# Kernel optimization log

Hardware: AMD Instinct MI355X
Metric: run time of the kernel (lower is better)

The kernel has to match this reference:

```python
import jax, jax.numpy as jnp
import numpy as np

D_MODEL = 1024
NUM_HEADS = 16
D_K = D_MODEL // NUM_HEADS
BATCH = 2
SEQ = 2048


def setup_inputs() -> dict:
    key = jax.random.key(0)
    ks = jax.random.split(key, 11)
    s = 1.0 / np.sqrt(D_MODEL)
    return {
        "query": jax.random.normal(ks[0], (BATCH, SEQ, D_MODEL), jnp.float32),
        "key_": jax.random.normal(ks[1], (BATCH, SEQ, D_MODEL), jnp.float32),
        "value": jax.random.normal(ks[2], (BATCH, SEQ, D_MODEL), jnp.float32),
        "w_q": jax.random.uniform(ks[3], (D_MODEL, D_MODEL), jnp.float32, -s, s),
        "b_q": jax.random.uniform(ks[4], (D_MODEL,), jnp.float32, -s, s),
        "w_k": jax.random.uniform(ks[5], (D_MODEL, D_MODEL), jnp.float32, -s, s),
        "b_k": jax.random.uniform(ks[6], (D_MODEL,), jnp.float32, -s, s),
        "w_v": jax.random.uniform(ks[7], (D_MODEL, D_MODEL), jnp.float32, -s, s),
        "b_v": jax.random.uniform(ks[8], (D_MODEL,), jnp.float32, -s, s),
        "w_o": jax.random.uniform(ks[9], (D_MODEL, D_MODEL), jnp.float32, -s, s),
        "b_o": jax.random.uniform(ks[10], (D_MODEL,), jnp.float32, -s, s),
    }


def reference(query, key_, value, w_q, b_q, w_k, b_k, w_v, b_v, w_o, b_o):
    B, S, D = query.shape
    H, dk = NUM_HEADS, D_K

    def proj(x, w, b):
        # torch Linear: x @ w.T + b ; reshape to (B, H, S, dk)
        return (x @ w.T + b).reshape(B, S, H, dk).transpose(0, 2, 1, 3)

    Q = proj(query, w_q, b_q)
    K = proj(key_, w_k, b_k)
    V = proj(value, w_v, b_v)

    scores = jnp.einsum("bhqd,bhkd->bhqk", Q, K) / jnp.sqrt(jnp.float32(dk))
    attn = jax.nn.softmax(scores, axis=-1)  # dropout is identity in eval
    ctx = jnp.einsum("bhqk,bhkd->bhqd", attn, V)
    ctx = ctx.transpose(0, 2, 1, 3).reshape(B, S, D)
    out = ctx @ w_o.T + b_o
    return out
```

## Files before the change

### kernel.cpp

```cpp
#include <hip/hip_runtime.h>
#include <cstdint>
#include <cstddef>

typedef unsigned short u16;
typedef short bf16x8 __attribute__((ext_vector_type(8)));
typedef unsigned short u16x8 __attribute__((ext_vector_type(8)));
typedef float f32x4 __attribute__((ext_vector_type(4)));

#define NHEAD 16
#define SEQ 2048
#define DMODEL 1024
#define BATCH 2
#define QSCALE 0.18033688011112042f

__device__ __forceinline__ float exp2_fast(float x) {
  return __builtin_amdgcn_exp2f(x);
}

__device__ __forceinline__ u16 f2bf(float f) {
  union { float f; unsigned u; } v; v.f = f;
  return (u16)((v.u + 0x7fffu + ((v.u >> 16) & 1u)) >> 16);
}

__device__ __forceinline__ unsigned cvt_pk(float a, float b) {
  unsigned r;
  asm("v_cvt_pk_bf16_f32 %0, %1, %2" : "=v"(r) : "v"(a), "v"(b));
  return r;
}

__device__ __forceinline__ int swz(int row, int colbyte) {
  return (row << 7) + (colbyte ^ ((row & 7) << 4));
}

__device__ __forceinline__ void load_lds16(const void* g, void* lds) {
  __builtin_amdgcn_global_load_lds(
      (const __attribute__((address_space(1))) unsigned int*)g,
      (__attribute__((address_space(3))) unsigned int*)lds, 16, 0, 0);
}

__global__ __launch_bounds__(256) void wconv(
    const float* __restrict__ wq, const float* __restrict__ wk,
    const float* __restrict__ wv, const float* __restrict__ wo,
    u16* __restrict__ Wq, u16* __restrict__ Wk, u16* __restrict__ Wv,
    u16* __restrict__ Wo) {
  int bid = blockIdx.x;
  int a = bid >> 9;
  int local = bid & 511;
  const float* in = a == 0 ? wq : a == 1 ? wk : a == 2 ? wv : wo;
  u16* out = a == 0 ? Wq : a == 1 ? Wk : a == 2 ? Wv : Wo;
  int i = local * 256 + threadIdx.x;
  const float4* p = (const float4*)in + (size_t)i * 2;
  float4 a4 = p[0], b4 = p[1];
  u16x8 o;
  o[0] = f2bf(a4.x); o[1] = f2bf(a4.y); o[2] = f2bf(a4.z); o[3] = f2bf(a4.w);
  o[4] = f2bf(b4.x); o[5] = f2bf(b4.y); o[6] = f2bf(b4.z); o[7] = f2bf(b4.w);
  *((u16x8*)out + i) = o;
}

__global__ __launch_bounds__(256) void gemm_qkv(
    const float* __restrict__ A0, const float* __restrict__ A1, const float* __restrict__ A2,
    const u16* __restrict__ W0, const u16* __restrict__ W1, const u16* __restrict__ W2,
    const float* __restrict__ b0, const float* __restrict__ b1, const float* __restrict__ b2,
    u16* __restrict__ C0, u16* __restrict__ C1, u16* __restrict__ C2) {
  constexpr int K = 1024;
  __shared__ u16 Ash[128 * 32];
  __shared__ u16 Bsh[128 * 32];
  const int z = blockIdx.z;
  const float* A = z == 0 ? A0 : z == 1 ? A1 : A2;
  const u16* W = z == 0 ? W0 : z == 1 ? W1 : W2;
  const float* bias = z == 0 ? b0 : z == 1 ? b1 : b2;
  u16* C = z == 0 ? C0 : z == 1 ? C1 : C2;
  const float scale = z == 0 ? QSCALE : 1.0f;

  const int t = threadIdx.x;
  const int w = t >> 6;
  const int l = t & 63;
  const int m0 = (blockIdx.x * 4 + (blockIdx.y >> 3)) * 128;
  const int n0 = (blockIdx.y & 7) * 128;
  const int wm = (w >> 1) * 64;
  const int wn = (w & 1) * 64;
  const int lr = l & 15;
  const int hi = l >> 4;
  const int lk = hi * 8;
  const int srow = l >> 2;
  const int scol = (l & 3) * 8;
  const int ar = t >> 2;
  const int ac = (t & 3) * 8;

  f32x4 acc[4][4] = {};

  for (int k0 = 0; k0 < K; k0 += 32) {
#pragma unroll
    for (int c = 0; c < 2; ++c) {
      int rb = (c * 4 + w) * 16 + srow;
      load_lds16(W + (size_t)(n0 + rb) * K + k0 + scol, &Bsh[(c * 4 + w) * 512]);
    }
    {
      const float* Af0 = A + (size_t)(m0 + ar) * K + k0 + ac;
      const float* Af1 = A + (size_t)(m0 + 64 + ar) * K + k0 + ac;
      f32x4 f0 = *(const f32x4*)&Af0[0];
      f32x4 f1 = *(const f32x4*)&Af0[4];
      f32x4 f2 = *(const f32x4*)&Af1[0];
      f32x4 f3 = *(const f32x4*)&Af1[4];
      uint4 o;
      o.x = cvt_pk(f0[0], f0[1]); o.y = cvt_pk(f0[2], f0[3]);
      o.z = cvt_pk(f1[0], f1[1]); o.w = cvt_pk(f1[2], f1[3]);
      *(uint4*)&Ash[ar * 32 + ac] = o;
      o.x = cvt_pk(f2[0], f2[1]); o.y = cvt_pk(f2[2], f2[3]);
      o.z = cvt_pk(f3[0], f3[1]); o.w = cvt_pk(f3[2], f3[3]);
      *(uint4*)&Ash[(64 + ar) * 32 + ac] = o;
    }
    __syncthreads();
    bf16x8 af[4], bfr[4];
#pragma unroll
    for (int i = 0; i < 4; ++i)
      af[i] = *(const bf16x8*)&Ash[(wm + i * 16 + lr) * 32 + lk];
#pragma unroll
    for (int j = 0; j < 4; ++j)
      bfr[j] = *(const bf16x8*)&Bsh[(wn + j * 16 + lr) * 32 + lk];
#pragma unroll
    for (int i = 0; i < 4; ++i)
#pragma unroll
      for (int j = 0; j < 4; ++j)
        acc[i][j] = __builtin_amdgcn_mfma_f32_16x16x32_bf16(af[i], bfr[j], acc[i][j], 0, 0, 0);
    __syncthreads();
  }

#pragma unroll
  for (int i = 0; i < 4; ++i)
#pragma unroll
    for (int j = 0; j < 4; ++j)
#pragma unroll
      for (int r = 0; r < 4; ++r) {
        int row = m0 + wm + i * 16 + hi * 4 + r;
        int col = n0 + wn + j * 16 + lr;
        float v = (acc[i][j][r] + bias[col]) * scale;
        int b = row >> 11, s = row & 2047;
        int h = col >> 6, d = col & 63;
        C[(((size_t)(b * NHEAD + h) * SEQ + s) << 6) + d] = f2bf(v);
      }
}

__global__ __launch_bounds__(256) void gemm_o(const u16* __restrict__ A,
                                              const u16* __restrict__ W,
                                              const float* __restrict__ bias,
                                              float* __restrict__ C) {
  constexpr int K = 1024;
  __shared__ u16 Ash[64 * 32];
  __shared__ u16 Bsh[128 * 32];
  const int t = threadIdx.x;
  const int w = t >> 6;
  const int l = t & 63;
  const int m0 = (blockIdx.x * 8 + (blockIdx.y >> 3)) * 64;
  const int n0 = (blockIdx.y & 7) * 128;
  const int wm = (w >> 1) * 32;
  const int wn = (w & 1) * 64;
  const int lr = l & 15;
  const int hi = l >> 4;
  const int lk = hi * 8;
  const int srow = l >> 2;
  const int scol = (l & 3) * 8;

  f32x4 acc[2][4] = {};

  for (int k0 = 0; k0 < K; k0 += 32) {
    {
      int ra = w * 16 + srow;
      load_lds16(A + (size_t)(m0 + ra) * K + k0 + scol, &Ash[w * 512]);
    }
#pragma unroll
    for (int c = 0; c < 2; ++c) {
      int rb = (c * 4 + w) * 16 + srow;
      load_lds16(W + (size_t)(n0 + rb) * K + k0 + scol, &Bsh[(c * 4 + w) * 512]);
    }
    __syncthreads();
    bf16x8 af[2], bfr[4];
#pragma unroll
    for (int i = 0; i < 2; ++i)
      af[i] = *(const bf16x8*)&Ash[(wm + i * 16 + lr) * 32 + lk];
#pragma unroll
    for (int j = 0; j < 4; ++j)
      bfr[j] = *(const bf16x8*)&Bsh[(wn + j * 16 + lr) * 32 + lk];
#pragma unroll
    for (int i = 0; i < 2; ++i)
#pragma unroll
      for (int j = 0; j < 4; ++j)
        acc[i][j] = __builtin_amdgcn_mfma_f32_16x16x32_bf16(af[i], bfr[j], acc[i][j], 0, 0, 0);
    __syncthreads();
  }

#pragma unroll
  for (int i = 0; i < 2; ++i)
#pragma unroll
    for (int j = 0; j < 4; ++j)
#pragma unroll
      for (int r = 0; r < 4; ++r) {
        int row = m0 + wm + i * 16 + hi * 4 + r;
        int col = n0 + wn + j * 16 + lr;
        C[(size_t)row * DMODEL + col] = acc[i][j][r] + bias[col];
      }
}

__global__ __launch_bounds__(256) void transpose_v(const u16* __restrict__ V,
                                                   u16* __restrict__ Vt) {
  __shared__ u16 tile[64][72];
  int st = blockIdx.x, bh = blockIdx.y;
  int t = threadIdx.x;
  {
    int s = t >> 2, part = (t & 3) * 16;
    const u16* g = V + (((size_t)bh * SEQ + st * 64 + s) << 6) + part;
    u16x8 v0 = *(const u16x8*)&g[0];
    u16x8 v1 = *(const u16x8*)&g[8];
    *(u16x8*)&tile[s][part] = v0;
    *(u16x8*)&tile[s][part + 8] = v1;
  }
  __syncthreads();
  {
    int d = t >> 2, sp = (t & 3) * 16;
    u16x8 o0, o1;
#pragma unroll
    for (int j = 0; j < 8; ++j) {
      int c0 = sp + j, c1 = sp + 8 + j;
      o0[j] = tile[(c0 & 3) * 16 + (c0 >> 2)][d];
      o1[j] = tile[(c1 & 3) * 16 + (c1 >> 2)][d];
    }
    u16* out = Vt + ((size_t)bh * 64 + d) * SEQ + st * 64 + sp;
    *(u16x8*)&out[0] = o0;
    *(u16x8*)&out[8] = o1;
  }
}

__device__ __forceinline__ void attn_tile(
    int kt, bool pf, const u16* Kg, const u16* Vg, int srow, int scb,
    char* QsB, char* KsC, char* VsC, char* KsN, char* VsN,
    bf16x8 (&qf)[2][2], f32x4 (&acc)[2][4], float (&lsum)[2][4],
    int w, int lr, int hi) {
  u16x8 nk0, nk1, nv0, nv1;
  if (pf) {
    const u16* kg = Kg + (kt + 1) * 4096;
    const u16* vg = Vg + (kt + 1) * 64;
    nk0 = *(const u16x8*)&kg[srow * 64 + scb / 2];
    nk1 = *(const u16x8*)&kg[srow * 64 + scb / 2 + 8];
    nv0 = *(const u16x8*)&vg[(size_t)srow * SEQ + scb / 2];
    nv1 = *(const u16x8*)&vg[(size_t)srow * SEQ + scb / 2 + 8];
  }

  f32x4 sc[2][4] = {};
  __builtin_amdgcn_s_setprio(1);
#pragma unroll
  for (int ks = 0; ks < 2; ++ks) {
    bf16x8 kb[4];
#pragma unroll
    for (int nt = 0; nt < 4; ++nt)
      kb[nt] = *(const bf16x8*)(KsC + swz(nt * 16 + lr, ks * 64 + hi * 16));
#pragma unroll
    for (int mt = 0; mt < 2; ++mt)
#pragma unroll
      for (int nt = 0; nt < 4; ++nt)
        sc[mt][nt] = __builtin_amdgcn_mfma_f32_16x16x32_bf16(qf[mt][ks], kb[nt], sc[mt][nt], 0, 0, 0);
  }
  __builtin_amdgcn_s_setprio(0);

#pragma unroll
  for (int mt = 0; mt < 2; ++mt)
#pragma unroll
    for (int r = 0; r < 4; ++r) {
      int prow = w * 32 + mt * 16 + hi * 4 + r;
      float p0 = exp2_fast(sc[mt][0][r]);
      float p1 = exp2_fast(sc[mt][1][r]);
      float p2 = exp2_fast(sc[mt][2][r]);
      float p3 = exp2_fast(sc[mt][3][r]);
      lsum[mt][r] += (p0 + p1) + (p2 + p3);
      uint2 pk;
      pk.x = cvt_pk(p0, p1);
      pk.y = cvt_pk(p2, p3);
      *(uint2*)(QsB + swz(prow, lr * 8)) = pk;
    }

  asm volatile("" ::: "memory");

  __builtin_amdgcn_s_setprio(1);
#pragma unroll
  for (int ks = 0; ks < 2; ++ks) {
    bf16x8 pa[2], vb[4];
#pragma unroll
    for (int mt = 0; mt < 2; ++mt)
      pa[mt] = *(const bf16x8*)(QsB + swz(w * 32 + mt * 16 + lr, ks * 64 + hi * 16));
#pragma unroll
    for (int nt = 0; nt < 4; ++nt)
      vb[nt] = *(const bf16x8*)(VsC + swz(nt * 16 + lr, ks * 64 + hi * 16));
#pragma unroll
    for (int mt = 0; mt < 2; ++mt)
#pragma unroll
      for (int nt = 0; nt < 4; ++nt)
        acc[mt][nt] = __builtin_amdgcn_mfma_f32_16x16x32_bf16(pa[mt], vb[nt], acc[mt][nt], 0, 0, 0);
  }
  __builtin_amdgcn_s_setprio(0);

  if (pf) {
    *(u16x8*)(KsN + swz(srow, scb)) = nk0;
    *(u16x8*)(KsN + swz(srow, scb + 16)) = nk1;
    *(u16x8*)(VsN + swz(srow, scb)) = nv0;
    *(u16x8*)(VsN + swz(srow, scb + 16)) = nv1;
  }
  __syncthreads();
}

__global__ __launch_bounds__(256) void attn(const u16* __restrict__ Q,
                                            const u16* __restrict__ K,
                                            const u16* __restrict__ Vt,
                                            u16* __restrict__ ctx) {
  __shared__ u16 Qs[128 * 64];
  __shared__ u16 Ks[2][64 * 64];
  __shared__ u16 Vs[2][64 * 64];
  char* const QsB = (char*)Qs;

  const int t = threadIdx.x, w = t >> 6, l = t & 63;
  const int lr = l & 15, hi = l >> 4;

  const int bid = blockIdx.x;
  const int idx = bid >> 3;
  const int bh = (bid & 7) * 4 + (idx >> 4);
  const int q0 = (idx & 15) * 128;

  const u16* Qg = Q + ((size_t)bh * SEQ + q0) * 64;
  const u16* Kg = K + (size_t)bh * SEQ * 64;
  const u16* Vg = Vt + (size_t)bh * 64 * SEQ;

#pragma unroll
  for (int i = 0; i < 4; ++i) {
    int c = i * 256 + t;
    int row = c >> 3, cb = (c & 7) * 16;
    u16x8 qv = *(const u16x8*)&Qg[row * 64 + cb / 2];
    *(u16x8*)(QsB + swz(row, cb)) = qv;
  }
  const int srow = t >> 2;
  const int scb = (t & 3) * 32;
  {
    u16x8 k0 = *(const u16x8*)&Kg[srow * 64 + scb / 2];
    u16x8 k1 = *(const u16x8*)&Kg[srow * 64 + scb / 2 + 8];
    u16x8 v0 = *(const u16x8*)&Vg[(size_t)srow * SEQ + scb / 2];
    u16x8 v1 = *(const u16x8*)&Vg[(size_t)srow * SEQ + scb / 2 + 8];
    char* KsB = (char*)Ks[0];
    char* VsB = (char*)Vs[0];
    *(u16x8*)(KsB + swz(srow, scb)) = k0;
    *(u16x8*)(KsB + swz(srow, scb + 16)) = k1;
    *(u16x8*)(VsB + swz(srow, scb)) = v0;
    *(u16x8*)(VsB + swz(srow, scb + 16)) = v1;
  }
  __syncthreads();

  bf16x8 qf[2][2];
#pragma unroll
  for (int mt = 0; mt < 2; ++mt)
#pragma unroll
    for (int ks = 0; ks < 2; ++ks)
      qf[mt][ks] = *(const bf16x8*)(QsB + swz(w * 32 + mt * 16 + lr, ks * 64 + hi * 16));

  f32x4 acc[2][4] = {};
  float lsum[2][4] = {{0.f, 0.f, 0.f, 0.f}, {0.f, 0.f, 0.f, 0.f}};

  for (int kt2 = 0; kt2 < SEQ / 128; ++kt2) {
    attn_tile(2 * kt2, true, Kg, Vg, srow, scb, QsB,
              (char*)Ks[0], (char*)Vs[0], (char*)Ks[1], (char*)Vs[1],
              qf, acc, lsum, w, lr, hi);
    attn_tile(2 * kt2 + 1, kt2 < SEQ / 128 - 1, Kg, Vg, srow, scb, QsB,
              (char*)Ks[1], (char*)Vs[1], (char*)Ks[0], (char*)Vs[0],
              qf, acc, lsum, w, lr, hi);
  }

  const int b = bh >> 4, h = bh & 15;
#pragma unroll
  for (int mt = 0; mt < 2; ++mt)
#pragma unroll
    for (int r = 0; r < 4; ++r) {
      float s = lsum[mt][r];
      s += __shfl_xor(s, 1);
      s += __shfl_xor(s, 2);
      s += __shfl_xor(s, 4);
      s += __shfl_xor(s, 8);
      float inv = 1.0f / s;
      int srow_ = q0 + w * 32 + mt * 16 + hi * 4 + r;
#pragma unroll
      for (int nt = 0; nt < 4; ++nt) {
        int d = nt * 16 + lr;
        ctx[((size_t)(b * SEQ + srow_)) * DMODEL + h * 64 + d] =
            f2bf(acc[mt][nt][r] * inv);
      }
    }
}

extern "C" void kernel_launch(void* const* d_in, const int* in_sizes, int n_in,
                              void* d_out, int out_size, void* d_ws, size_t ws_size,
                              hipStream_t stream) {
  const float* q  = (const float*)d_in[0];
  const float* k  = (const float*)d_in[1];
  const float* v  = (const float*)d_in[2];
  const float* wq = (const float*)d_in[3];
  const float* bq = (const float*)d_in[4];
  const float* wk = (const float*)d_in[5];
  const float* bk = (const float*)d_in[6];
  const float* wv = (const float*)d_in[7];
  const float* bv = (const float*)d_in[8];
  const float* wo = (const float*)d_in[9];
  const float* bo = (const float*)d_in[10];

  const size_t XB = (size_t)4096 * 1024 * 2;
  const size_t WB = (size_t)1024 * 1024 * 2;
  char* ws = (char*)d_ws;
  u16* ctxb = (u16*)(ws);
  u16* Vtb = (u16*)(ws + XB);
  u16* Wq = (u16*)(ws + 3 * XB);
  u16* Wk = (u16*)(ws + 3 * XB + WB);
  u16* Wv = (u16*)(ws + 3 * XB + 2 * WB);
  u16* Wo = (u16*)(ws + 3 * XB + 3 * WB);
  u16* Qb = (u16*)(ws + 4 * XB);
  u16* Kb = (u16*)(ws + 5 * XB);
  u16* Vb = (u16*)(ws + 6 * XB);

  wconv<<<2048, 256, 0, stream>>>(wq, wk, wv, wo, Wq, Wk, Wv, Wo);

  gemm_qkv<<<dim3(8, 32, 3), 256, 0, stream>>>(q, k, v, Wq, Wk, Wv,
                                               bq, bk, bv, Qb, Kb, Vb);

  transpose_v<<<dim3(SEQ / 64, BATCH * NHEAD), 256, 0, stream>>>(Vb, Vtb);

  attn<<<512, 256, 0, stream>>>(Qb, Kb, Vtb, ctxb);

  gemm_o<<<dim3(8, 64), 256, 0, stream>>>(ctxb, Wo, bo, (float*)d_out);
}
```

Before: 119.0 us.

## Swizzle LDS tiles in projection GEMMs and prefetch fp32 A tile

Applies an XOR swizzle to the LDS column layout of the A and B tiles in both the QKV projection and output projection GEMMs, matching the global source offsets for the direct-to-LDS loads and the fragment reads, to reduce LDS bank conflicts. In the QKV GEMM, the fp32 activation loads for the next k-step are issued before the barrier so global latency overlaps the MFMA work. The cost is more live registers for the prefetched data, and correctness depends on the swizzle on the load side and the read side staying consistent.

```diff
diff --git a/kernel.cpp b/kernel.cpp
--- a/kernel.cpp
+++ b/kernel.cpp
@@ -84,40 +84,50 @@
   const int lk = hi * 8;
   const int srow = l >> 2;
   const int scol = (l & 3) * 8;
+  const int ssw = ((l >> 3) & 3) << 3;
   const int ar = t >> 2;
   const int ac = (t & 3) * 8;
+  const int asw = ((ar >> 1) & 3) << 3;
+  const int fsw = ((lr >> 1) & 3) << 3;
 
   f32x4 acc[4][4] = {};
+
+  const float* Abase0 = A + (size_t)(m0 + ar) * K;
+  const float* Abase1 = A + (size_t)(m0 + 64 + ar) * K;
+  f32x4 f0 = *(const f32x4*)&Abase0[ac];
+  f32x4 f1 = *(const f32x4*)&Abase0[ac + 4];
+  f32x4 f2 = *(const f32x4*)&Abase1[ac];
+  f32x4 f3 = *(const f32x4*)&Abase1[ac + 4];
 
   for (int k0 = 0; k0 < K; k0 += 32) {
 #pragma unroll
     for (int c = 0; c < 2; ++c) {
       int rb = (c * 4 + w) * 16 + srow;
-      load_lds16(W + (size_t)(n0 + rb) * K + k0 + scol, &Bsh[(c * 4 + w) * 512]);
+      load_lds16(W + (size_t)(n0 + rb) * K + k0 + (scol ^ ssw), &Bsh[(c * 4 + w) * 512]);
     }
     {
-      const float* Af0 = A + (size_t)(m0 + ar) * K + k0 + ac;
-      const float* Af1 = A + (size_t)(m0 + 64 + ar) * K + k0 + ac;
-      f32x4 f0 = *(const f32x4*)&Af0[0];
-      f32x4 f1 = *(const f32x4*)&Af0[4];
-      f32x4 f2 = *(const f32x4*)&Af1[0];
-      f32x4 f3 = *(const f32x4*)&Af1[4];
       uint4 o;
       o.x = cvt_pk(f0[0], f0[1]); o.y = cvt_pk(f0[2], f0[3]);
       o.z = cvt_pk(f1[0], f1[1]); o.w = cvt_pk(f1[2], f1[3]);
-      *(uint4*)&Ash[ar * 32 + ac] = o;
+      *(uint4*)&Ash[ar * 32 + (ac ^ asw)] = o;
       o.x = cvt_pk(f2[0], f2[1]); o.y = cvt_pk(f2[2], f2[3]);
       o.z = cvt_pk(f3[0], f3[1]); o.w = cvt_pk(f3[2], f3[3]);
-      *(uint4*)&Ash[(64 + ar) * 32 + ac] = o;
+      *(uint4*)&Ash[(64 + ar) * 32 + (ac ^ asw)] = o;
+    }
+    if (k0 + 32 < K) {
+      f0 = *(const f32x4*)&Abase0[k0 + 32 + ac];
+      f1 = *(const f32x4*)&Abase0[k0 + 32 + ac + 4];
+      f2 = *(const f32x4*)&Abase1[k0 + 32 + ac];
+      f3 = *(const f32x4*)&Abase1[k0 + 32 + ac + 4];
     }
     __syncthreads();
     bf16x8 af[4], bfr[4];
 #pragma unroll
     for (int i = 0; i < 4; ++i)
-      af[i] = *(const bf16x8*)&Ash[(wm + i * 16 + lr) * 32 + lk];
+      af[i] = *(const bf16x8*)&Ash[(wm + i * 16 + lr) * 32 + (lk ^ fsw)];
 #pragma unroll
     for (int j = 0; j < 4; ++j)
-      bfr[j] = *(const bf16x8*)&Bsh[(wn + j * 16 + lr) * 32 + lk];
+      bfr[j] = *(const bf16x8*)&Bsh[(wn + j * 16 + lr) * 32 + (lk ^ fsw)];
 #pragma unroll
     for (int i = 0; i < 4; ++i)
 #pragma unroll
@@ -160,27 +170,29 @@
   const int lk = hi * 8;
   const int srow = l >> 2;
   const int scol = (l & 3) * 8;
+  const int ssw = ((l >> 3) & 3) << 3;
+  const int fsw = ((lr >> 1) & 3) << 3;
 
   f32x4 acc[2][4] = {};
 
   for (int k0 = 0; k0 < K; k0 += 32) {
     {
       int ra = w * 16 + srow;
-      load_lds16(A + (size_t)(m0 + ra) * K + k0 + scol, &Ash[w * 512]);
+      load_lds16(A + (size_t)(m0 + ra) * K + k0 + (scol ^ ssw), &Ash[w * 512]);
     }
 #pragma unroll
     for (int c = 0; c < 2; ++c) {
       int rb = (c * 4 + w) * 16 + srow;
-      load_lds16(W + (size_t)(n0 + rb) * K + k0 + scol, &Bsh[(c * 4 + w) * 512]);
+      load_lds16(W + (size_t)(n0 + rb) * K + k0 + (scol ^ ssw), &Bsh[(c * 4 + w) * 512]);
     }
     __syncthreads();
     bf16x8 af[2], bfr[4];
 #pragma unroll
     for (int i = 0; i < 2; ++i)
-      af[i] = *(const bf16x8*)&Ash[(wm + i * 16 + lr) * 32 + lk];
+      af[i] = *(const bf16x8*)&Ash[(wm + i * 16 + lr) * 32 + (lk ^ fsw)];
 #pragma unroll
     for (int j = 0; j < 4; ++j)
-      bfr[j] = *(const bf16x8*)&Bsh[(wn + j * 16 + lr) * 32 + lk];
+      bfr[j] = *(const bf16x8*)&Bsh[(wn + j * 16 + lr) * 32 + (lk ^ fsw)];
 #pragma unroll
     for (int i = 0; i < 2; ++i)
 #pragma unroll
```

Measured after the change: 117.5 us, median of 2. Within noise of the previous version (-1.3%).
